# Kernel tuning notes

Hardware: AMD Instinct MI355X
Metric: run time of the kernel (lower is better)

Reference implementation:

```python
import jax, jax.numpy as jnp
import numpy as np

MUL = 128                  # multiplicity of each irrep slot in in1 / out
Z = 100000                 # batch (e.g. number of edges)
L = [0, 1]                 # l of irrep slot i; dims are 2l+1 -> [1, 3]
INSTR = [(0, 0, 0), (0, 1, 1), (1, 0, 1), (1, 1, 0)]  # parity-allowed 'uvw' paths


def _w3j_np(l1, l2, l3):
    """Real-basis Wigner-3j (e3nn convention) for l <= 1."""
    if (l1, l2, l3) == (0, 0, 0):
        return np.ones((1, 1, 1))
    e = np.eye(3) / np.sqrt(3.0)
    if (l1, l2, l3) == (1, 1, 0):
        return e[:, :, None]
    if (l1, l2, l3) == (0, 1, 1):
        return e[None, :, :]
    if (l1, l2, l3) == (1, 0, 1):
        return e[:, None, :]
    raise ValueError((l1, l2, l3))


# fan-in per output slot for component-normalized path weights
FAN_IN = {0: 0, 1: 0}
for (_i1, _i2, _io) in INSTR:
    FAN_IN[_io] += MUL * 1  # mul_in1 * mul_in2 for 'uvw'

WEIGHT_NUMEL = len(INSTR) * MUL * 1 * MUL  # 65536


def setup_inputs() -> dict:
    key = jax.random.key(0)
    k1, k2, k3 = jax.random.split(key, 3)
    x1 = jax.random.normal(k1, (Z, MUL * 1 + MUL * 3), jnp.float32)   # 128x0e + 128x1o
    x2 = jax.random.normal(k2, (Z, 1 + 3), jnp.float32)               # 1x0e + 1x1o
    weights = jax.random.normal(k3, (WEIGHT_NUMEL,), jnp.float32)     # shared 'uvw' weights
    return {"x1": x1, "x2": x2, "weights": weights}


def _tensor_product(x1, x2, weights):
    z = x1.shape[0]
    # split flat features into (mul, 2l+1) segments
    x1s = [x1[:, :MUL].reshape(z, MUL, 1), x1[:, MUL:].reshape(z, MUL, 3)]
    x2s = [x2[:, :1].reshape(z, 1, 1), x2[:, 1:].reshape(z, 1, 3)]
    outs = [jnp.zeros((z, MUL, 1), x1.dtype), jnp.zeros((z, MUL, 3), x1.dtype)]
    off = 0
    for (i1, i2, io) in INSTR:
        nw = MUL * 1 * MUL
        w = weights[off:off + nw].reshape(MUL, 1, MUL)  # (u, v, w)
        off += nw
        C = jnp.asarray(_w3j_np(L[i1], L[i2], L[io]), x1.dtype)
        pw = jnp.asarray(np.sqrt(2 * L[io] + 1.0) / np.sqrt(FAN_IN[io]), x1.dtype)
        # segmented CG contraction: small (i,j,k) dims, large z,u,w dims
        tmp = jnp.einsum('zui,zvj,ijk->zuvk', x1s[i1], x2s[i2], C)
        outs[io] = outs[io] + pw * jnp.einsum('zuvk,uvw->zwk', tmp, w)
    return jnp.concatenate([o.reshape(z, -1) for o in outs], axis=1)


def reference(x1, x2, weights):
    return _tensor_product(x1, x2, weights)
```

## Files before the change

kernel.cpp:

```cpp
#include <hip/hip_runtime.h>


#define Z_TOTAL   100000
#define BM        32
#define NTILES_Z  (Z_TOTAL / BM)
#define GRID      256
#define THREADS   512

using bf16x8 = __attribute__((ext_vector_type(8))) __bf16;
using f32x4  = __attribute__((ext_vector_type(4))) float;

struct __align__(4) F3 { float x, y, z; };

struct TileRegs {
    float4 b;
    float4 a0a, a0b;
    float4 a1[6];
};

__device__ __forceinline__ void bar_lds() {
    __builtin_amdgcn_sched_barrier(0);
    asm volatile("s_waitcnt lgkmcnt(0)");
    __builtin_amdgcn_s_barrier();
    __builtin_amdgcn_sched_barrier(0);
}

__device__ __forceinline__ int lds_idx(int row, int chunk) {
    return row * 256 + ((chunk ^ (row & 7)) << 3);
}

__device__ __forceinline__ void tile_load(TileRegs& T, const float* __restrict__ x1,
                                          const float* __restrict__ x2,
                                          int z0, int zl, int u0) {
    const float* xr = x1 + (size_t)(z0 + zl) * 512;
    T.b   = *(const float4*)(x2 + (size_t)(z0 + zl) * 4);
    T.a0a = *(const float4*)(xr + u0);
    T.a0b = *(const float4*)(xr + u0 + 4);
    #pragma unroll
    for (int i = 0; i < 6; ++i)
        T.a1[i] = *(const float4*)(xr + 128 + u0 * 3 + i * 4);
}

__device__ __forceinline__ void tile_stage(const TileRegs& T, unsigned short* lds,
                                           int zl, int ug) {
    const float b0 = T.b.x, b1x = T.b.y, b1y = T.b.z, b1z = T.b.w;
    const float a0[8] = {T.a0a.x, T.a0a.y, T.a0a.z, T.a0a.w,
                         T.a0b.x, T.a0b.y, T.a0b.z, T.a0b.w};
    bf16x8 pk;
    #pragma unroll
    for (int i = 0; i < 8; ++i) pk[i] = (__bf16)(b0 * a0[i]);
    *(bf16x8*)&lds[lds_idx(zl, ug)] = pk;
    #pragma unroll
    for (int i = 0; i < 8; ++i) pk[i] = (__bf16)(b1x * a0[i]);
    *(bf16x8*)&lds[lds_idx(32 + zl, ug)] = pk;
    #pragma unroll
    for (int i = 0; i < 8; ++i) pk[i] = (__bf16)(b1y * a0[i]);
    *(bf16x8*)&lds[lds_idx(64 + zl, ug)] = pk;
    #pragma unroll
    for (int i = 0; i < 8; ++i) pk[i] = (__bf16)(b1z * a0[i]);
    *(bf16x8*)&lds[lds_idx(96 + zl, ug)] = pk;

    float a1[24];
    #pragma unroll
    for (int i = 0; i < 6; ++i) {
        a1[i*4+0] = T.a1[i].x; a1[i*4+1] = T.a1[i].y;
        a1[i*4+2] = T.a1[i].z; a1[i*4+3] = T.a1[i].w;
    }
    #pragma unroll
    for (int i = 0; i < 8; ++i)
        pk[i] = (__bf16)(a1[3*i]*b1x + a1[3*i+1]*b1y + a1[3*i+2]*b1z);
    *(bf16x8*)&lds[lds_idx(zl, 16 + ug)] = pk;
    #pragma unroll
    for (int i = 0; i < 8; ++i) pk[i] = (__bf16)(b0 * a1[3*i + 0]);
    *(bf16x8*)&lds[lds_idx(32 + zl, 16 + ug)] = pk;
    #pragma unroll
    for (int i = 0; i < 8; ++i) pk[i] = (__bf16)(b0 * a1[3*i + 1]);
    *(bf16x8*)&lds[lds_idx(64 + zl, 16 + ug)] = pk;
    #pragma unroll
    for (int i = 0; i < 8; ++i) pk[i] = (__bf16)(b0 * a1[3*i + 2]);
    *(bf16x8*)&lds[lds_idx(96 + zl, 16 + ug)] = pk;
}

__device__ __forceinline__ void mfma_store(const unsigned short* lds,
                                           const bf16x8 Bf[2][8],
                                           float* __restrict__ out,
                                           int z0, int m16, int q, int n) {
    #pragma unroll
    for (int m2 = 0; m2 < 2; ++m2) {
        f32x4 acc = {0.f, 0.f, 0.f, 0.f};
        const int r = m2 * 16 + m16;
        #pragma unroll
        for (int kt = 0; kt < 8; ++kt) {
            const bf16x8 a = *(const bf16x8*)&lds[lds_idx(r, kt * 4 + q)];
            acc = __builtin_amdgcn_mfma_f32_16x16x32_bf16(a, Bf[0][kt], acc, 0, 0, 0);
        }
        #pragma unroll
        for (int reg = 0; reg < 4; ++reg) {
            const int z = z0 + m2 * 16 + q * 4 + reg;
            out[(size_t)z * 512 + n] = acc[reg];
        }
    }
    #pragma unroll
    for (int zt = 0; zt < 2; ++zt) {
        f32x4 a3[3];
        #pragma unroll
        for (int k3 = 0; k3 < 3; ++k3) {
            a3[k3] = (f32x4){0.f, 0.f, 0.f, 0.f};
            const int r = 32 + k3 * 32 + zt * 16 + m16;
            #pragma unroll
            for (int kt = 0; kt < 8; ++kt) {
                const bf16x8 a = *(const bf16x8*)&lds[lds_idx(r, kt * 4 + q)];
                a3[k3] = __builtin_amdgcn_mfma_f32_16x16x32_bf16(a, Bf[1][kt], a3[k3], 0, 0, 0);
            }
        }
        #pragma unroll
        for (int reg = 0; reg < 4; ++reg) {
            const int z = z0 + zt * 16 + q * 4 + reg;
            F3 v; v.x = a3[0][reg]; v.y = a3[1][reg]; v.z = a3[2][reg];
            *(F3*)(out + (size_t)z * 512 + 128 + n * 3) = v;
        }
    }
}

__global__ __launch_bounds__(THREADS, 2)
void tp_kernel(const float* __restrict__ x1, const float* __restrict__ x2,
               const float* __restrict__ wts, float* __restrict__ out)
{
    __shared__ __align__(16) unsigned short lds[128 * 256];

    const int t    = threadIdx.x;
    const int lane = t & 63;
    const int wv   = t >> 6;
    const int m16  = lane & 15;
    const int q    = lane >> 4;

    const float S16 = 0.0625f;
    const float S48 = 0.0625f * 0.57735026918962576f;
    bf16x8 Bf[2][8];
    {
        const int n = wv * 16 + m16;
        #pragma unroll
        for (int mat = 0; mat < 2; ++mat) {
            #pragma unroll
            for (int kt = 0; kt < 8; ++kt) {
                bf16x8 bb;
                #pragma unroll
                for (int j = 0; j < 8; ++j) {
                    const int k = kt * 32 + q * 8 + j;
                    float v;
                    if (mat == 0) {
                        v = (k < 128) ? wts[k * 128 + n] * S16
                                      : wts[49152 + (k - 128) * 128 + n] * S48;
                    } else {
                        v = (k < 128) ? wts[16384 + k * 128 + n] * S16
                                      : wts[32768 + (k - 128) * 128 + n] * S16;
                    }
                    bb[j] = (__bf16)v;
                }
                Bf[mat][kt] = bb;
            }
        }
    }

    const int zl = t >> 4;
    const int ug = t & 15;
    const int u0 = ug * 8;
    const int n  = wv * 16 + m16;

    int tile = blockIdx.x;
    TileRegs P, N;
    tile_load(P, x1, x2, tile * BM, zl, u0);

    for (;;) {
        int nx = tile + GRID;
        bar_lds();
        tile_stage(P, lds, zl, ug);
        bar_lds();
        if (nx < NTILES_Z)
            tile_load(N, x1, x2, nx * BM, zl, u0);
        mfma_store(lds, Bf, out, tile * BM, m16, q, n);
        if (nx >= NTILES_Z) return;
        tile = nx;

        nx = tile + GRID;
        bar_lds();
        tile_stage(N, lds, zl, ug);
        bar_lds();
        if (nx < NTILES_Z)
            tile_load(P, x1, x2, nx * BM, zl, u0);
        mfma_store(lds, Bf, out, tile * BM, m16, q, n);
        if (nx >= NTILES_Z) return;
        tile = nx;
    }
}

extern "C" void kernel_launch(void* const* d_in, const int* in_sizes, int n_in,
                              void* d_out, int out_size, void* d_ws, size_t ws_size,
                              hipStream_t stream) {
    (void)in_sizes; (void)n_in; (void)d_ws; (void)ws_size; (void)out_size;
    const float* x1  = (const float*)d_in[0];
    const float* x2  = (const float*)d_in[1];
    const float* wts = (const float*)d_in[2];
    float* out = (float*)d_out;
    tp_kernel<<<dim3(GRID), dim3(THREADS), 0, stream>>>(x1, x2, wts, out);
}
```

Measured before the change: 357.2 us.

## Drop register prefetch double-buffering and raise occupancy to four blocks per CU

Removes the software pipelining that prefetched the next tile's x1/x2 into registers during the MFMA phase. Each tile is now loaded and staged synchronously, and occupancy doubles (launch bounds 4, grid 512) to hide latency across blocks instead of within one. This frees the registers that held the prefetch buffers, but each block now stalls on global loads and relies on other resident blocks to cover them. LDS use per block (64KB) may limit how many blocks can actually be resident.

```diff
diff --git a/kernel.cpp b/kernel.cpp
--- a/kernel.cpp
+++ b/kernel.cpp
@@ -4,19 +4,13 @@
 #define Z_TOTAL   100000
 #define BM        32
 #define NTILES_Z  (Z_TOTAL / BM)
-#define GRID      256
+#define GRID      512
 #define THREADS   512
 
 using bf16x8 = __attribute__((ext_vector_type(8))) __bf16;
 using f32x4  = __attribute__((ext_vector_type(4))) float;
 
 struct __align__(4) F3 { float x, y, z; };
-
-struct TileRegs {
-    float4 b;
-    float4 a0a, a0b;
-    float4 a1[6];
-};
 
 __device__ __forceinline__ void bar_lds() {
     __builtin_amdgcn_sched_barrier(0);
@@ -29,23 +23,21 @@
     return row * 256 + ((chunk ^ (row & 7)) << 3);
 }
 
-__device__ __forceinline__ void tile_load(TileRegs& T, const float* __restrict__ x1,
-                                          const float* __restrict__ x2,
-                                          int z0, int zl, int u0) {
-    const float* xr = x1 + (size_t)(z0 + zl) * 512;
-    T.b   = *(const float4*)(x2 + (size_t)(z0 + zl) * 4);
-    T.a0a = *(const float4*)(xr + u0);
-    T.a0b = *(const float4*)(xr + u0 + 4);
+__device__ __forceinline__ void tile_stage(const float* __restrict__ xr,
+                                           const float* __restrict__ x2r,
+                                           unsigned short* lds, int zl, int ug) {
+    const int u0 = ug * 8;
+    const float4 b4  = *(const float4*)x2r;
+    const float4 a0a = *(const float4*)(xr + u0);
+    const float4 a0b = *(const float4*)(xr + u0 + 4);
+    float4 a1v[6];
     #pragma unroll
     for (int i = 0; i < 6; ++i)
-        T.a1[i] = *(const float4*)(xr + 128 + u0 * 3 + i * 4);
-}
+        a1v[i] = *(const float4*)(xr + 128 + u0 * 3 + i * 4);
+    __builtin_amdgcn_sched_barrier(0);
 
-__device__ __forceinline__ void tile_stage(const TileRegs& T, unsigned short* lds,
-                                           int zl, int ug) {
-    const float b0 = T.b.x, b1x = T.b.y, b1y = T.b.z, b1z = T.b.w;
-    const float a0[8] = {T.a0a.x, T.a0a.y, T.a0a.z, T.a0a.w,
-                         T.a0b.x, T.a0b.y, T.a0b.z, T.a0b.w};
+    const float b0 = b4.x, b1x = b4.y, b1y = b4.z, b1z = b4.w;
+    const float a0[8] = {a0a.x, a0a.y, a0a.z, a0a.w, a0b.x, a0b.y, a0b.z, a0b.w};
     bf16x8 pk;
     #pragma unroll
     for (int i = 0; i < 8; ++i) pk[i] = (__bf16)(b0 * a0[i]);
@@ -63,8 +55,8 @@
     float a1[24];
     #pragma unroll
     for (int i = 0; i < 6; ++i) {
-        a1[i*4+0] = T.a1[i].x; a1[i*4+1] = T.a1[i].y;
-        a1[i*4+2] = T.a1[i].z; a1[i*4+3] = T.a1[i].w;
+        a1[i*4+0] = a1v[i].x; a1[i*4+1] = a1v[i].y;
+        a1[i*4+2] = a1v[i].z; a1[i*4+3] = a1v[i].w;
     }
     #pragma unroll
     for (int i = 0; i < 8; ++i)
@@ -122,7 +114,7 @@
     }
 }
 
-__global__ __launch_bounds__(THREADS, 2)
+__global__ __launch_bounds__(THREADS, 4)
 void tp_kernel(const float* __restrict__ x1, const float* __restrict__ x2,
                const float* __restrict__ wts, float* __restrict__ out)
 {
@@ -164,33 +156,15 @@
 
     const int zl = t >> 4;
     const int ug = t & 15;
-    const int u0 = ug * 8;
     const int n  = wv * 16 + m16;
 
-    int tile = blockIdx.x;
-    TileRegs P, N;
-    tile_load(P, x1, x2, tile * BM, zl, u0);
-
-    for (;;) {
-        int nx = tile + GRID;
+    for (int tile = blockIdx.x; tile < NTILES_Z; tile += GRID) {
+        const int z0 = tile * BM;
         bar_lds();
-        tile_stage(P, lds, zl, ug);
+        tile_stage(x1 + (size_t)(z0 + zl) * 512,
+                   x2 + (size_t)(z0 + zl) * 4, lds, zl, ug);
         bar_lds();
-        if (nx < NTILES_Z)
-            tile_load(N, x1, x2, nx * BM, zl, u0);
-        mfma_store(lds, Bf, out, tile * BM, m16, q, n);
-        if (nx >= NTILES_Z) return;
-        tile = nx;
-
-        nx = tile + GRID;
-        bar_lds();
-        tile_stage(N, lds, zl, ug);
-        bar_lds();
-        if (nx < NTILES_Z)
-            tile_load(P, x1, x2, nx * BM, zl, u0);
-        mfma_store(lds, Bf, out, tile * BM, m16, q, n);
-        if (nx >= NTILES_Z) return;
-        tile = nx;
+        mfma_store(lds, Bf, out, z0, m16, q, n);
     }
 }
 
```

New measurement: 355.5 us. Within noise of the previous version (-0.5%).
